# Optimization experiments

Hardware: AMD Instinct MI355X
Metric: run time of the kernel (lower is better)

Reference implementation:

```python
import jax, jax.numpy as jnp
import numpy as np

DECAY = 0.99
EPS = 1e-05
N, K, D = 32768, 8192, 64


def setup_inputs() -> dict:
    key = jax.random.key(0)
    k1, k2, k3 = jax.random.split(key, 3)
    return {
        "inputs": jax.random.normal(k1, (N, D), dtype=jnp.float32),
        "embedding_w": jax.random.normal(k2, (K, D), dtype=jnp.float32),
        "ema_w": jax.random.normal(k3, (K, D), dtype=jnp.float32),
        "ema_cluster_size": jnp.zeros((K,), dtype=jnp.float32),
    }


def reference(inputs, embedding_w, ema_w, ema_cluster_size):
    k = embedding_w.shape[0]
    # pairwise squared L2 distances: [N, K]
    distances = (
        jnp.sum(inputs ** 2, axis=1, keepdims=True)
        + jnp.sum(embedding_w ** 2, axis=1)
        - 2.0 * inputs @ embedding_w.T
    )
    encoding_indices = jnp.argmin(distances, axis=1)           # [N] int
    encodings = jax.nn.one_hot(encoding_indices, k, dtype=inputs.dtype)  # [N, K]
    codebook = embedding_w  # returned codebook is the PRE-update weight (as in torch source)

    # EMA updates (training branch), expressed functionally
    cluster_size = ema_cluster_size * DECAY + (1.0 - DECAY) * jnp.sum(encodings, axis=0)
    n = jnp.sum(cluster_size)
    cluster_size = (cluster_size + EPS) / (n + k * EPS) * n
    dw = encodings.T @ inputs                                   # [K, D]
    ema_w_new = ema_w * DECAY + (1.0 - DECAY) * dw
    embedding_new = ema_w_new / cluster_size[:, None]

    return (encodings, codebook, cluster_size, ema_w_new, embedding_new)
```

## Files before the change

### kernel.cpp

```cpp
#include <hip/hip_runtime.h>
#include <hip/hip_bf16.h>

#define N_PTS 32768
#define K_CLU 8192
#define D_DIM 64
#define DECAYF 0.99f
#define OMDF   0.01f
#define EPSF   1e-5f

typedef _Float16 v8h __attribute__((ext_vector_type(8)));
typedef float    v4f __attribute__((ext_vector_type(4)));

#define OFF_IDX    0
#define OFF_COUNTS (131072)
#define OFF_DW     (131072 + 32768)
#define OFF_NSUM   (OFF_DW + 2097152)
#define OFF_EHI    (OFF_NSUM + 16)
#define OFF_ELO    (OFF_EHI + 1048576)
#define OFF_E2     (OFF_ELO + 1048576)
#define WS_NEEDED  (OFF_E2 + 32768)

__global__ __launch_bounds__(256) void vq_prep(
    const float* __restrict__ emb, const float* __restrict__ ema_cs,
    _Float16* __restrict__ ehi, _Float16* __restrict__ elo,
    float* __restrict__ e2, float* __restrict__ nsum)
{
    const int wave = threadIdx.x >> 6;
    const int lane = threadIdx.x & 63;
    if (blockIdx.x < 2048) {
        const int row = blockIdx.x * 4 + wave;
        float v = emb[(size_t)row * D_DIM + lane];
        _Float16 h = (_Float16)v;
        _Float16 l = (_Float16)(v - (float)h);
        ehi[(size_t)row * D_DIM + lane] = h;
        elo[(size_t)row * D_DIM + lane] = l;
        float s = v * v;
        #pragma unroll
        for (int m = 1; m < 64; m <<= 1) s += __shfl_xor(s, m, 64);
        if (lane == 0) e2[row] = s;
    } else {
        const int t = (blockIdx.x - 2048) * 256 + threadIdx.x;
        float v = ema_cs[t];
        #pragma unroll
        for (int m = 1; m < 64; m <<= 1) v += __shfl_xor(v, m, 64);
        if (lane == 0) atomicAdd(nsum, v);
    }
}

__global__ __launch_bounds__(256) void vq_main(
    const float* __restrict__ x,
    const _Float16* __restrict__ ehi, const _Float16* __restrict__ elo,
    const float* __restrict__ e2,
    float* __restrict__ enc,
    int* __restrict__ idx_out,
    unsigned int* __restrict__ counts,
    float* __restrict__ dw)
{
    __shared__ _Float16 sEhi[128 * 72];
    __shared__ _Float16 sElo[128 * 72];
    __shared__ float    sE2[128];

    const unsigned bid = blockIdx.x;
    if ((bid & 3u) != 0u) {
        const unsigned zid = bid - bid / 4u - 1u;
        const size_t nvec = (size_t)N_PTS * K_CLU / 4;
        v4f z = {0.f, 0.f, 0.f, 0.f};
        v4f* enc4 = (v4f*)enc;
        for (size_t v = (size_t)zid * 256 + threadIdx.x; v < nvec; v += 768u * 256u)
            __builtin_nontemporal_store(z, enc4 + v);
        return;
    }

    const unsigned cb = bid >> 2;
    const int wave = threadIdx.x >> 6;
    const int lane = threadIdx.x & 63;
    const int quad = lane >> 4;
    const int l15  = lane & 15;
    const int ptbase = cb * 128 + wave * 32;

    v8h xh[2][2], xl[2][2];
    #pragma unroll
    for (int g = 0; g < 2; ++g) {
        const int pt = ptbase + g * 16 + l15;
        const float* xp = x + (size_t)pt * D_DIM + quad * 8;
        #pragma unroll
        for (int c = 0; c < 2; ++c) {
            float4 a = *(const float4*)(xp + c * 32);
            float4 b = *(const float4*)(xp + c * 32 + 4);
            float vv[8] = {a.x, a.y, a.z, a.w, b.x, b.y, b.z, b.w};
            v8h hh, ll;
            #pragma unroll
            for (int j = 0; j < 8; ++j) {
                _Float16 h = (_Float16)vv[j];
                hh[j] = h;
                ll[j] = (_Float16)(vv[j] - (float)h);
            }
            xh[g][c] = hh; xl[g][c] = ll;
        }
    }

    float best[8]; int bidx[8];
    #pragma unroll
    for (int i = 0; i < 8; ++i) { best[i] = 3.4e38f; bidx[i] = 0; }

    for (int chunk = 0; chunk < 64; ++chunk) {
        const int kbase = chunk * 128;
        __syncthreads();
        {
            const uint4* gh = (const uint4*)(ehi + (size_t)kbase * D_DIM);
            const uint4* gl = (const uint4*)(elo + (size_t)kbase * D_DIM);
            #pragma unroll
            for (int it = 0; it < 4; ++it) {
                int u = threadIdx.x + 256 * it;
                int row = u >> 3, uc = u & 7;
                *(uint4*)&sEhi[row * 72 + uc * 8] = gh[row * 8 + uc];
                *(uint4*)&sElo[row * 72 + uc * 8] = gl[row * 8 + uc];
            }
            if (threadIdx.x < 128) sE2[threadIdx.x] = e2[kbase + threadIdx.x];
        }
        __syncthreads();

        #pragma unroll
        for (int sub = 0; sub < 8; ++sub) {
            const int nl = sub * 16 + l15;
            v8h bh0 = *(const v8h*)&sEhi[nl * 72 + quad * 8];
            v8h bh1 = *(const v8h*)&sEhi[nl * 72 + 32 + quad * 8];
            v8h bl0 = *(const v8h*)&sElo[nl * 72 + quad * 8];
            v8h bl1 = *(const v8h*)&sElo[nl * 72 + 32 + quad * 8];
            const float e2v = sE2[nl];
            const int kidx = kbase + nl;
            #pragma unroll
            for (int g = 0; g < 2; ++g) {
                v4f acc = {0.f, 0.f, 0.f, 0.f};
                acc = __builtin_amdgcn_mfma_f32_16x16x32_f16(xh[g][0], bh0, acc, 0, 0, 0);
                acc = __builtin_amdgcn_mfma_f32_16x16x32_f16(xh[g][1], bh1, acc, 0, 0, 0);
                acc = __builtin_amdgcn_mfma_f32_16x16x32_f16(xl[g][0], bh0, acc, 0, 0, 0);
                acc = __builtin_amdgcn_mfma_f32_16x16x32_f16(xl[g][1], bh1, acc, 0, 0, 0);
                acc = __builtin_amdgcn_mfma_f32_16x16x32_f16(xh[g][0], bl0, acc, 0, 0, 0);
                acc = __builtin_amdgcn_mfma_f32_16x16x32_f16(xh[g][1], bl1, acc, 0, 0, 0);
                #pragma unroll
                for (int r = 0; r < 4; ++r) {
                    float dist = fmaf(acc[r], -2.0f, e2v);
                    if (dist < best[g * 4 + r]) { best[g * 4 + r] = dist; bidx[g * 4 + r] = kidx; }
                }
            }
        }
    }

    #pragma unroll
    for (int i = 0; i < 8; ++i) {
        #pragma unroll
        for (int m = 1; m < 16; m <<= 1) {
            float ov = __shfl_xor(best[i], m, 64);
            int   oi = __shfl_xor(bidx[i], m, 64);
            if (ov < best[i] || (ov == best[i] && oi < bidx[i])) { best[i] = ov; bidx[i] = oi; }
        }
    }

    if (l15 == 0) {
        #pragma unroll
        for (int g = 0; g < 2; ++g)
            #pragma unroll
            for (int r = 0; r < 4; ++r) {
                int p = ptbase + g * 16 + quad * 4 + r;
                idx_out[p] = bidx[g * 4 + r];
                atomicAdd(&counts[bidx[g * 4 + r]], 1u);
            }
    }

    #pragma unroll
    for (int j = 0; j < 32; ++j) {
        const int g = j >> 4, row = j & 15;
        const int src = (row >> 2) * 16;
        const int r = row & 3;
        int k = __shfl(bidx[g * 4 + r], src, 64);
        float val = x[(size_t)(ptbase + j) * D_DIM + lane];
        atomicAdd(&dw[(size_t)k * D_DIM + lane], val);
    }
}

__global__ __launch_bounds__(256) void vq_finalize(
    const float* __restrict__ emb, const float* __restrict__ ema_w,
    const float* __restrict__ ema_cs,
    const unsigned int* __restrict__ counts, const float* __restrict__ dw,
    const float* __restrict__ nsum, const int* __restrict__ idx,
    float* __restrict__ out)
{
    const size_t ENC = (size_t)N_PTS * K_CLU;
    float* out_codebook = out + ENC;
    float* out_cs       = out_codebook + (size_t)K_CLU * D_DIM;
    float* out_ema      = out_cs + K_CLU;
    float* out_emb      = out_ema + (size_t)K_CLU * D_DIM;

    if (blockIdx.x < 2048) {
        const int gid = blockIdx.x * 256 + threadIdx.x;
        const int k = gid >> 6, d = gid & 63;
        float dwv = dw[gid];
        float en  = DECAYF * ema_w[gid] + OMDF * dwv;
        float cnt = (float)counts[k];
        float cs_raw = DECAYF * ema_cs[k] + OMDF * cnt;
        float n  = DECAYF * nsum[0] + OMDF * (float)N_PTS;
        float cs = (cs_raw + EPSF) / (n + (float)K_CLU * EPSF) * n;
        out_codebook[gid] = emb[gid];
        out_ema[gid] = en;
        out_emb[gid] = en / cs;
        if (d == 0) out_cs[k] = cs;
    } else {
        const int i = (blockIdx.x - 2048) * 256 + threadIdx.x;
        out[(size_t)i * K_CLU + idx[i]] = 1.0f;
    }
}

extern "C" void kernel_launch(void* const* d_in, const int* in_sizes, int n_in,
                              void* d_out, int out_size, void* d_ws, size_t ws_size,
                              hipStream_t stream)
{
    const float* x      = (const float*)d_in[0];
    const float* emb    = (const float*)d_in[1];
    const float* ema_w  = (const float*)d_in[2];
    const float* ema_cs = (const float*)d_in[3];
    float* out = (float*)d_out;
    char* ws = (char*)d_ws;

    int*          idx    = (int*)(ws + OFF_IDX);
    unsigned int* counts = (unsigned int*)(ws + OFF_COUNTS);
    float*        dw     = (float*)(ws + OFF_DW);
    float*        nsum   = (float*)(ws + OFF_NSUM);
    _Float16*     ehi    = (_Float16*)(ws + OFF_EHI);
    _Float16*     elo    = (_Float16*)(ws + OFF_ELO);
    float*        e2     = (float*)(ws + OFF_E2);

    hipMemsetAsync(ws + OFF_COUNTS, 0, (OFF_NSUM + 16) - OFF_COUNTS, stream);

    vq_prep<<<2080, 256, 0, stream>>>(emb, ema_cs, ehi, elo, e2, nsum);
    vq_main<<<1024, 256, 0, stream>>>(x, ehi, elo, e2, out, idx, counts, dw);
    vq_finalize<<<2176, 256, 0, stream>>>(emb, ema_w, ema_cs, counts, dw, nsum, idx, out);
}
```

Before: 1.273 ms.

## Interleave one-hot zero-fill into distance loop and halve points per block

Removes the separate zero-fill blocks and has every compute block write its own slice of the encodings buffer with nontemporal stores inside each chunk iteration, so the store traffic overlaps the MFMA distance work. Each wave now handles 16 points instead of 32, giving 512 blocks of 64 points. This halves codebook reuse per shared-memory load, so total LDS and global reads of the codebook double, and the grid gets smaller. The aim is to hide the 1 GB zero-write behind compute instead of having it compete with compute blocks.

```diff
diff --git a/kernel.cpp b/kernel.cpp
--- a/kernel.cpp
+++ b/kernel.cpp
@@ -18,7 +18,6 @@
 #define OFF_EHI    (OFF_NSUM + 16)
 #define OFF_ELO    (OFF_EHI + 1048576)
 #define OFF_E2     (OFF_ELO + 1048576)
-#define WS_NEEDED  (OFF_E2 + 32768)
 
 __global__ __launch_bounds__(256) void vq_prep(
     const float* __restrict__ emb, const float* __restrict__ ema_cs,
@@ -47,7 +46,7 @@
     }
 }
 
-__global__ __launch_bounds__(256) void vq_main(
+__global__ __launch_bounds__(256) void vq_fused(
     const float* __restrict__ x,
     const _Float16* __restrict__ ehi, const _Float16* __restrict__ elo,
     const float* __restrict__ e2,
@@ -60,28 +59,17 @@
     __shared__ _Float16 sElo[128 * 72];
     __shared__ float    sE2[128];
 
-    const unsigned bid = blockIdx.x;
-    if ((bid & 3u) != 0u) {
-        const unsigned zid = bid - bid / 4u - 1u;
-        const size_t nvec = (size_t)N_PTS * K_CLU / 4;
-        v4f z = {0.f, 0.f, 0.f, 0.f};
-        v4f* enc4 = (v4f*)enc;
-        for (size_t v = (size_t)zid * 256 + threadIdx.x; v < nvec; v += 768u * 256u)
-            __builtin_nontemporal_store(z, enc4 + v);
-        return;
-    }
-
-    const unsigned cb = bid >> 2;
-    const int wave = threadIdx.x >> 6;
-    const int lane = threadIdx.x & 63;
+    const int bid  = blockIdx.x;
+    const int tid  = threadIdx.x;
+    const int wave = tid >> 6;
+    const int lane = tid & 63;
     const int quad = lane >> 4;
     const int l15  = lane & 15;
-    const int ptbase = cb * 128 + wave * 32;
-
-    v8h xh[2][2], xl[2][2];
-    #pragma unroll
-    for (int g = 0; g < 2; ++g) {
-        const int pt = ptbase + g * 16 + l15;
+    const int ptbase = bid * 64 + wave * 16;
+
+    v8h xh[2], xl[2];
+    {
+        const int pt = ptbase + l15;
         const float* xp = x + (size_t)pt * D_DIM + quad * 8;
         #pragma unroll
         for (int c = 0; c < 2; ++c) {
@@ -95,13 +83,17 @@
                 hh[j] = h;
                 ll[j] = (_Float16)(vv[j] - (float)h);
             }
-            xh[g][c] = hh; xl[g][c] = ll;
-        }
-    }
-
-    float best[8]; int bidx[8];
+            xh[c] = hh; xl[c] = ll;
+        }
+    }
+
+    float best[4]; int bidx4[4];
     #pragma unroll
-    for (int i = 0; i < 8; ++i) { best[i] = 3.4e38f; bidx[i] = 0; }
+    for (int i = 0; i < 4; ++i) { best[i] = 3.4e38f; bidx4[i] = 0; }
+
+    v4f* enc4 = (v4f*)enc;
+    const size_t zbase = (size_t)bid * 131072 + tid;
+    const v4f zz = {0.f, 0.f, 0.f, 0.f};
 
     for (int chunk = 0; chunk < 64; ++chunk) {
         const int kbase = chunk * 128;
@@ -111,14 +103,21 @@
             const uint4* gl = (const uint4*)(elo + (size_t)kbase * D_DIM);
             #pragma unroll
             for (int it = 0; it < 4; ++it) {
-                int u = threadIdx.x + 256 * it;
+                int u = tid + 256 * it;
                 int row = u >> 3, uc = u & 7;
                 *(uint4*)&sEhi[row * 72 + uc * 8] = gh[row * 8 + uc];
                 *(uint4*)&sElo[row * 72 + uc * 8] = gl[row * 8 + uc];
             }
-            if (threadIdx.x < 128) sE2[threadIdx.x] = e2[kbase + threadIdx.x];
+            if (tid < 128) sE2[tid] = e2[kbase + tid];
         }
         __syncthreads();
+
+        {
+            const size_t zo = zbase + (size_t)chunk * 2048;
+            #pragma unroll
+            for (int it = 0; it < 8; ++it)
+                __builtin_nontemporal_store(zz, enc4 + zo + it * 256);
+        }
 
         #pragma unroll
         for (int sub = 0; sub < 8; ++sub) {
@@ -129,51 +128,45 @@
             v8h bl1 = *(const v8h*)&sElo[nl * 72 + 32 + quad * 8];
             const float e2v = sE2[nl];
             const int kidx = kbase + nl;
-            #pragma unroll
-            for (int g = 0; g < 2; ++g) {
-                v4f acc = {0.f, 0.f, 0.f, 0.f};
-                acc = __builtin_amdgcn_mfma_f32_16x16x32_f16(xh[g][0], bh0, acc, 0, 0, 0);
-                acc = __builtin_amdgcn_mfma_f32_16x16x32_f16(xh[g][1], bh1, acc, 0, 0, 0);
-                acc = __builtin_amdgcn_mfma_f32_16x16x32_f16(xl[g][0], bh0, acc, 0, 0, 0);
-                acc = __builtin_amdgcn_mfma_f32_16x16x32_f16(xl[g][1], bh1, acc, 0, 0, 0);
-                acc = __builtin_amdgcn_mfma_f32_16x16x32_f16(xh[g][0], bl0, acc, 0, 0, 0);
-                acc = __builtin_amdgcn_mfma_f32_16x16x32_f16(xh[g][1], bl1, acc, 0, 0, 0);
-                #pragma unroll
-                for (int r = 0; r < 4; ++r) {
-                    float dist = fmaf(acc[r], -2.0f, e2v);
-                    if (dist < best[g * 4 + r]) { best[g * 4 + r] = dist; bidx[g * 4 + r] = kidx; }
-                }
+            v4f acc = {0.f, 0.f, 0.f, 0.f};
+            acc = __builtin_amdgcn_mfma_f32_16x16x32_f16(xh[0], bh0, acc, 0, 0, 0);
+            acc = __builtin_amdgcn_mfma_f32_16x16x32_f16(xh[1], bh1, acc, 0, 0, 0);
+            acc = __builtin_amdgcn_mfma_f32_16x16x32_f16(xl[0], bh0, acc, 0, 0, 0);
+            acc = __builtin_amdgcn_mfma_f32_16x16x32_f16(xl[1], bh1, acc, 0, 0, 0);
+            acc = __builtin_amdgcn_mfma_f32_16x16x32_f16(xh[0], bl0, acc, 0, 0, 0);
+            acc = __builtin_amdgcn_mfma_f32_16x16x32_f16(xh[1], bl1, acc, 0, 0, 0);
+            #pragma unroll
+            for (int r = 0; r < 4; ++r) {
+                float dist = fmaf(acc[r], -2.0f, e2v);
+                if (dist < best[r]) { best[r] = dist; bidx4[r] = kidx; }
             }
         }
     }
 
     #pragma unroll
-    for (int i = 0; i < 8; ++i) {
+    for (int i = 0; i < 4; ++i) {
         #pragma unroll
         for (int m = 1; m < 16; m <<= 1) {
             float ov = __shfl_xor(best[i], m, 64);
-            int   oi = __shfl_xor(bidx[i], m, 64);
-            if (ov < best[i] || (ov == best[i] && oi < bidx[i])) { best[i] = ov; bidx[i] = oi; }
+            int   oi = __shfl_xor(bidx4[i], m, 64);
+            if (ov < best[i] || (ov == best[i] && oi < bidx4[i])) { best[i] = ov; bidx4[i] = oi; }
         }
     }
 
     if (l15 == 0) {
         #pragma unroll
-        for (int g = 0; g < 2; ++g)
-            #pragma unroll
-            for (int r = 0; r < 4; ++r) {
-                int p = ptbase + g * 16 + quad * 4 + r;
-                idx_out[p] = bidx[g * 4 + r];
-                atomicAdd(&counts[bidx[g * 4 + r]], 1u);
-            }
+        for (int r = 0; r < 4; ++r) {
+            int p = ptbase + quad * 4 + r;
+            idx_out[p] = bidx4[r];
+            atomicAdd(&counts[bidx4[r]], 1u);
+        }
     }
 
     #pragma unroll
-    for (int j = 0; j < 32; ++j) {
-        const int g = j >> 4, row = j & 15;
-        const int src = (row >> 2) * 16;
-        const int r = row & 3;
-        int k = __shfl(bidx[g * 4 + r], src, 64);
+    for (int j = 0; j < 16; ++j) {
+        const int src = (j >> 2) * 16;
+        const int r = j & 3;
+        int k = __shfl(bidx4[r], src, 64);
         float val = x[(size_t)(ptbase + j) * D_DIM + lane];
         atomicAdd(&dw[(size_t)k * D_DIM + lane], val);
     }
@@ -233,6 +226,6 @@
     hipMemsetAsync(ws + OFF_COUNTS, 0, (OFF_NSUM + 16) - OFF_COUNTS, stream);
 
     vq_prep<<<2080, 256, 0, stream>>>(emb, ema_cs, ehi, elo, e2, nsum);
-    vq_main<<<1024, 256, 0, stream>>>(x, ehi, elo, e2, out, idx, counts, dw);
+    vq_fused<<<512, 256, 0, stream>>>(x, ehi, elo, e2, out, idx, counts, dw);
     vq_finalize<<<2176, 256, 0, stream>>>(emb, ema_w, ema_cs, counts, dw, nsum, idx, out);
 }
```

New measurement: 1.086 ms. 14.7% less time.
